# Performance work log

Hardware: AMD Instinct MI355X
Metric: run time of the kernel (lower is better)

The kernel has to match this reference:

```python
import jax, jax.numpy as jnp
import numpy as np
from jax import lax

B, T, E, H, V = 1024, 128, 300, 100, 50000
K = 4  # topk in catch()
NEG_INF = -1e30


def setup_inputs() -> dict:
    key = jax.random.key(0)
    ks = jax.random.split(key, 12)
    word_id = jax.random.randint(ks[0], (B, T), 0, V, dtype=jnp.int32)
    sen_len = jax.random.randint(ks[1], (B,), K, T + 1, dtype=jnp.int32)  # >= K for topk
    label_word_id = jax.random.randint(ks[2], (B, 1), 0, V, dtype=jnp.int32)
    emb = jax.random.normal(ks[3], (V, E), jnp.float32) * 0.1
    W_ih = jax.random.normal(ks[4], (4 * H, E), jnp.float32) * 0.05
    W_hh = jax.random.normal(ks[5], (4 * H, H), jnp.float32) * 0.05
    b_ih = jax.random.normal(ks[6], (4 * H,), jnp.float32) * 0.05
    b_hh = jax.random.normal(ks[7], (4 * H,), jnp.float32) * 0.05
    lin_W = jax.random.normal(ks[8], (6, H), jnp.float32) * 0.1
    lin_b = jax.random.normal(ks[9], (6,), jnp.float32) * 0.1
    ll_W = jax.random.normal(ks[10], (H, E), jnp.float32) * 0.05
    ll_b = jax.random.normal(ks[11], (H,), jnp.float32) * 0.05
    return dict(word_id=word_id, sen_len=sen_len, label_word_id=label_word_id,
                emb=emb, W_ih=W_ih, W_hh=W_hh, b_ih=b_ih, b_hh=b_hh,
                lin_W=lin_W, lin_b=lin_b, ll_W=ll_W, ll_b=ll_b)


def _lstm(x, W_ih, W_hh, b_ih, b_hh):
    # x: (B, T, E) -> out: (B, T, H). Single layer, pytorch gate order i,f,g,o.
    b = b_ih + b_hh
    def step(carry, x_t):
        h, c = carry
        gates = x_t @ W_ih.T + h @ W_hh.T + b  # (B, 4H)
        i, f, g, o = jnp.split(gates, 4, axis=-1)
        c = jax.nn.sigmoid(f) * c + jax.nn.sigmoid(i) * jnp.tanh(g)
        h = jax.nn.sigmoid(o) * jnp.tanh(c)
        return (h, c), h
    h0 = jnp.zeros((x.shape[0], W_hh.shape[1]), x.dtype)
    (_, _), hs = lax.scan(step, (h0, h0), x.transpose(1, 0, 2))
    return hs.transpose(1, 0, 2)


def reference(word_id, sen_len, label_word_id, emb, W_ih, W_hh, b_ih, b_hh,
              lin_W, lin_b, ll_W, ll_b):
    word_vec = emb[word_id]                      # (B, T, E)
    out = _lstm(word_vec, W_ih, W_hh, b_ih, b_hh)  # (B, T, H)

    # last valid hidden state -> linear
    last = out[jnp.arange(out.shape[0]), sen_len - 1]  # (B, H)
    out_f = last @ lin_W.T + lin_b               # (B, 6)

    # label vector through llinear
    label_vec = emb[label_word_id[:, 0]] @ ll_W.T + ll_b  # (B, H)

    # --- catch(), vectorized ---
    scores = jnp.einsum('bth,bh->bt', out, label_vec)     # (B, T)
    valid = jnp.arange(out.shape[1])[None, :] < sen_len[:, None]  # (B, T)
    vals, idx = lax.top_k(jnp.where(valid, scores, NEG_INF), K)   # (B, K)
    s_value = jnp.take_along_axis(out, idx[:, :, None], axis=1)   # (B, K, H)
    pos = jnp.sum(s_value * vals[:, :, None], axis=1)             # (B, H)

    # neg: valid positions excluding topk; original bug: vector_list accumulates
    # across the batch loop -> cumulative sum over batch dimension.
    top_mask = jnp.zeros(valid.shape, bool).at[
        jnp.arange(valid.shape[0])[:, None], idx].set(True)
    neg_mask = valid & ~top_mask                                   # (B, T)
    per_neg = jnp.einsum('bth,bt->bh', out, neg_mask.astype(out.dtype))
    neg = jnp.cumsum(per_neg, axis=0)                              # (B, H)

    l_rep = pos @ lin_W.T + lin_b
    r_rep = neg @ lin_W.T + lin_b
    return (out_f, l_rep, r_rep)
```

## Files before the change

### kernel.cpp

```cpp
#include <hip/hip_runtime.h>
#include <hip/hip_bf16.h>
#include <cstdint>

#define Bn   1024
#define Tn   128
#define En   300
#define Hn   100
#define Vn   50000
#define G4n  400
#define MPn  50048
#define NPn  448

typedef __bf16 bf16x8 __attribute__((ext_vector_type(8)));
typedef _Float16 half8 __attribute__((ext_vector_type(8)));
typedef _Float16 half2v __attribute__((ext_vector_type(2)));
typedef float  f32x4  __attribute__((ext_vector_type(4)));

#define OFF_TABLE  0ull
#define OFF_WFRAG  44800000ull
#define OFF_WFRAGB 44914688ull
#define OFF_PN6    45201408ull

__device__ __forceinline__ float sigf(float x) {
    return __builtin_amdgcn_rcpf(1.0f + __expf(-x));
}
__device__ __forceinline__ float tanhfast(float x) {
    return 1.0f - 2.0f * __builtin_amdgcn_rcpf(__expf(2.0f * x) + 1.0f);
}

#define BAR_LDS() do {                                         \
    asm volatile("s_waitcnt lgkmcnt(0)" ::: "memory");          \
    __builtin_amdgcn_s_barrier();                               \
    asm volatile("" ::: "memory");                              \
} while (0)

#define DPP_ADD_SHL(v, N) do {                                                     \
    int _s = __builtin_amdgcn_update_dpp(0, __builtin_bit_cast(int, (v)),          \
                                         0x100 | (N), 0xF, 0xF, true);             \
    (v) += __builtin_bit_cast(float, _s);                                          \
} while (0)

__global__ void k_prep(const float* __restrict__ W_ih, const float* __restrict__ W_hh,
                       uint4* __restrict__ wfrag, uint4* __restrict__ wfragB) {
    int idx = blockIdx.x * 256 + threadIdx.x;
    if (idx < 28 * 4 * 64) {
        int lane = idx & 63, tk = idx >> 6;
        int nt = tk >> 2, kc = tk & 3;
        int n = nt * 16 + (lane & 15);
        int k0 = kc * 32 + (lane >> 4) * 8;
        int q = n & 3, u = n >> 2;
        union { _Float16 h[8]; uint4 v; } pk;
#pragma unroll
        for (int j = 0; j < 8; j++) {
            int k = k0 + j;
            pk.h[j] = (_Float16)((u < Hn && k < Hn) ? W_hh[(size_t)(q * Hn + u) * Hn + k] : 0.0f);
        }
        wfrag[idx] = pk.v;
    }
    if (idx < 10 * 28 * 64) {
        int lane = idx & 63, tk = idx >> 6;
        int kc = tk / 28, nsg = tk - kc * 28;
        int n = nsg * 16 + (lane & 15);
        int k0 = kc * 32 + (lane >> 4) * 8;
        int q = n & 3, u = n >> 2;
        union { __bf16 h[8]; uint4 v; } pk;
#pragma unroll
        for (int j = 0; j < 8; j++) {
            int k = k0 + j;
            pk.h[j] = (__bf16)((u < Hn && k < En) ? W_ih[(size_t)(q * Hn + u) * En + k] : 0.0f);
        }
        wfragB[idx] = pk.v;
    }
}

__global__ __launch_bounds__(256, 2) void k_table(
    const float* __restrict__ emb, const uint4* __restrict__ wfragB,
    const float* __restrict__ b_ih, const float* __restrict__ b_hh,
    _Float16* __restrict__ table) {
    __shared__ __bf16 a_sh[64][328];
    const int tid = threadIdx.x;
    const int mt = blockIdx.x >> 1, nh = blockIdx.x & 1;

#pragma unroll
    for (int it = 0; it < 5; it++) {
        int x = it * 256 + tid;
        int row = x / 20, seg = x - row * 20;
        int gr = mt * 64 + row;
        const float* ar = emb + (size_t)(gr < Vn ? gr : Vn - 1) * En;
        int c0 = seg * 16;
        union { __bf16 h[16]; bf16x8 v[2]; } pk;
#pragma unroll
        for (int g = 0; g < 4; g++) {
            int c = c0 + g * 4;
            if (c + 4 <= En) {
                float4 f = *(const float4*)(ar + c);
                pk.h[g * 4 + 0] = (__bf16)f.x; pk.h[g * 4 + 1] = (__bf16)f.y;
                pk.h[g * 4 + 2] = (__bf16)f.z; pk.h[g * 4 + 3] = (__bf16)f.w;
            } else {
                pk.h[g * 4 + 0] = (__bf16)0.f; pk.h[g * 4 + 1] = (__bf16)0.f;
                pk.h[g * 4 + 2] = (__bf16)0.f; pk.h[g * 4 + 3] = (__bf16)0.f;
            }
        }
        *(bf16x8*)&a_sh[row][c0] = pk.v[0];
        *(bf16x8*)&a_sh[row][c0 + 8] = pk.v[1];
    }
    __syncthreads();

    const int wv = tid >> 6, l = tid & 63;
    const int c16 = l & 15, quad = l >> 4;
    f32x4 acc[14];
#pragma unroll
    for (int i = 0; i < 14; i++) acc[i] = (f32x4){0.f, 0.f, 0.f, 0.f};

    uint4 bcur[14];
#pragma unroll
    for (int ns = 0; ns < 14; ns++) bcur[ns] = wfragB[((0 * 28 + nh * 14 + ns) << 6) + l];

    for (int kc = 0; kc < 10; kc++) {
        uint4 bnxt[14];
        if (kc < 9) {
#pragma unroll
            for (int ns = 0; ns < 14; ns++) bnxt[ns] = wfragB[(((kc + 1) * 28 + nh * 14 + ns) << 6) + l];
        }
        bf16x8 af = *(const bf16x8*)&a_sh[wv * 16 + c16][kc * 32 + quad * 8];
#pragma unroll
        for (int ns = 0; ns < 14; ns++)
            acc[ns] = __builtin_amdgcn_mfma_f32_16x16x32_bf16(af, __builtin_bit_cast(bf16x8, bcur[ns]), acc[ns], 0, 0, 0);
        if (kc < 9) {
#pragma unroll
            for (int ns = 0; ns < 14; ns++) bcur[ns] = bnxt[ns];
        }
    }
#pragma unroll
    for (int ns = 0; ns < 14; ns++) {
        int n = (nh * 14 + ns) * 16 + c16;
        int q = n & 3, u = n >> 2;
        if (u < Hn) {
            int j = q * Hn + u;
            float bias = b_ih[j] + b_hh[j];
#pragma unroll
            for (int r = 0; r < 4; r++) {
                int m = mt * 64 + wv * 16 + quad * 4 + r;
                if (m < Vn) table[(size_t)m * NPn + n] = (_Float16)(acc[ns][r] + bias);
            }
        }
    }
}

__global__ __launch_bounds__(512, 2) void k_lstm(
    const int* __restrict__ word_id, const int* __restrict__ sen_len,
    const int* __restrict__ lwid, const float* __restrict__ emb,
    const float* __restrict__ llW, const float* __restrict__ llb,
    const _Float16* __restrict__ table, const uint4* __restrict__ wfrag,
    const float* __restrict__ linW, const float* __restrict__ linb,
    float* __restrict__ pn6, float* __restrict__ d_out) {
    __shared__ __align__(16) _Float16 h_cur[2][4][144];
    __shared__ __align__(16) _Float16 oh_lds[4][12832];
    __shared__ __align__(16) float    spw[4][Tn][16];
    __shared__ int      widc[4][Tn];
    __shared__ float    pos_sh[4][Hn];
    __shared__ float    lasth_sh[4][Hn];
    __shared__ float    neg_sh[4][Hn];
    __shared__ float    tk_val[4][4];
    __shared__ int      tk_idx[4][4];

    const int tid = threadIdx.x;
    const int w = tid >> 6, l = tid & 63;
    const int c16 = l & 15, quad = l >> 4;
    const int b0 = blockIdx.x * 4;

    for (int i = tid; i < 576; i += 512) ((uint32_t*)h_cur)[i] = 0u;
    { int imb = tid >> 7, it = tid & 127; widc[imb][it] = word_id[(b0 + imb) * Tn + it] * NPn; }

    const bool has4 = (w == 0);
    const int TB = has4 ? 0 : 4 + 3 * (w - 1);
    const int NT = has4 ? 4 : 3;

    half8 bfr[4][4];
#pragma unroll
    for (int kc = 0; kc < 4; kc++) {
        bfr[0][kc] = __builtin_bit_cast(half8, wfrag[((TB + 0) * 4 + kc) * 64 + l]);
        bfr[1][kc] = __builtin_bit_cast(half8, wfrag[((TB + 1) * 4 + kc) * 64 + l]);
        bfr[2][kc] = __builtin_bit_cast(half8, wfrag[((TB + 2) * 4 + kc) * 64 + l]);
        if (has4) bfr[3][kc] = __builtin_bit_cast(half8, wfrag[((TB + 3) * 4 + kc) * 64 + l]);
    }

    const int mb = c16 & 3, dup = c16 >> 2;
    const bool act = (dup < NT);
    const int u = (TB + dup) * 4 + quad;
    const int slen = act ? sen_len[b0 + mb] : 0;
    const _Float16* tb_u = table + u * 4;

    float lt_reg = 0.f;
    if (act) {
        const int lid = lwid[b0 + mb];
        const float* er = emb + (size_t)lid * En;
        const float* wr = llW + (size_t)u * En;
        float sx = 0.f, sy = 0.f, sz = 0.f, sw = 0.f;
        for (int k = 0; k < En; k += 4) {
            float4 e = *(const float4*)(er + k);
            float4 ww = *(const float4*)(wr + k);
            sx += e.x * ww.x; sy += e.y * ww.y;
            sz += e.z * ww.z; sw += e.w * ww.w;
        }
        lt_reg = (sx + sy) + (sz + sw) + llb[u];
    }

    __syncthreads();

    uint2 xq = {0, 0}, xq1 = {0, 0};
    if (act) {
        xq  = *(const uint2*)(tb_u + (size_t)widc[mb][0]);
        xq1 = *(const uint2*)(tb_u + (size_t)widc[mb][1]);
    }

    float c_reg = 0.f, sumh = 0.f, lasth = 0.f;
    float p_carry = 0.f;

    for (int t = 0; t < Tn; t++) {
        const _Float16* hp = &h_cur[t & 1][0][0];
        half8 hf0 = *(const half8*)(hp + (c16 & 3) * 144 + 0 * 32 + quad * 8);
        half8 hf1 = *(const half8*)(hp + (c16 & 3) * 144 + 1 * 32 + quad * 8);
        half8 hf2 = *(const half8*)(hp + (c16 & 3) * 144 + 2 * 32 + quad * 8);
        half8 hf3 = *(const half8*)(hp + (c16 & 3) * 144 + 3 * 32 + quad * 8);
        f32x4 acc0, acc1, acc2, acc3;
        acc0 = __builtin_amdgcn_mfma_f32_16x16x32_f16(bfr[0][0], hf0, (f32x4){0.f, 0.f, 0.f, 0.f}, 0, 0, 0);
        acc1 = __builtin_amdgcn_mfma_f32_16x16x32_f16(bfr[1][0], hf0, (f32x4){0.f, 0.f, 0.f, 0.f}, 0, 0, 0);
        acc2 = __builtin_amdgcn_mfma_f32_16x16x32_f16(bfr[2][0], hf0, (f32x4){0.f, 0.f, 0.f, 0.f}, 0, 0, 0);
        if (has4) acc3 = __builtin_amdgcn_mfma_f32_16x16x32_f16(bfr[3][0], hf0, (f32x4){0.f, 0.f, 0.f, 0.f}, 0, 0, 0);
        acc0 = __builtin_amdgcn_mfma_f32_16x16x32_f16(bfr[0][1], hf1, acc0, 0, 0, 0);
        acc1 = __builtin_amdgcn_mfma_f32_16x16x32_f16(bfr[1][1], hf1, acc1, 0, 0, 0);
        acc2 = __builtin_amdgcn_mfma_f32_16x16x32_f16(bfr[2][1], hf1, acc2, 0, 0, 0);
        if (has4) acc3 = __builtin_amdgcn_mfma_f32_16x16x32_f16(bfr[3][1], hf1, acc3, 0, 0, 0);
        acc0 = __builtin_amdgcn_mfma_f32_16x16x32_f16(bfr[0][2], hf2, acc0, 0, 0, 0);
        acc1 = __builtin_amdgcn_mfma_f32_16x16x32_f16(bfr[1][2], hf2, acc1, 0, 0, 0);
        acc2 = __builtin_amdgcn_mfma_f32_16x16x32_f16(bfr[2][2], hf2, acc2, 0, 0, 0);
        if (has4) acc3 = __builtin_amdgcn_mfma_f32_16x16x32_f16(bfr[3][2], hf2, acc3, 0, 0, 0);
        acc0 = __builtin_amdgcn_mfma_f32_16x16x32_f16(bfr[0][3], hf3, acc0, 0, 0, 0);
        acc1 = __builtin_amdgcn_mfma_f32_16x16x32_f16(bfr[1][3], hf3, acc1, 0, 0, 0);
        acc2 = __builtin_amdgcn_mfma_f32_16x16x32_f16(bfr[2][3], hf3, acc2, 0, 0, 0);
        if (has4) acc3 = __builtin_amdgcn_mfma_f32_16x16x32_f16(bfr[3][3], hf3, acc3, 0, 0, 0);
        {
            float pr = p_carry;
            DPP_ADD_SHL(pr, 4);
            DPP_ADD_SHL(pr, 8);
            int sw_ = __builtin_amdgcn_ds_swizzle(__builtin_bit_cast(int, pr), 0x401F);
            pr += __builtin_bit_cast(float, sw_);
            if (c16 < 4 && (quad & 1) == 0 && t > 0)
                spw[c16][t - 1][w * 2 + (quad >> 1)] = pr;
        }
        f32x4 g = acc0;
        g = (dup == 1) ? acc1 : g;
        g = (dup == 2) ? acc2 : g;
        if (has4) g = (dup == 3) ? acc3 : g;
        float p = 0.f;
        if (act) {
            half2v x01 = __builtin_bit_cast(half2v, xq.x);
            half2v x23 = __builtin_bit_cast(half2v, xq.y);
            float gi = g[0] + (float)x01.x;
            float gf = g[1] + (float)x01.y;
            float gg = g[2] + (float)x23.x;
            float go = g[3] + (float)x23.y;
            float c = sigf(gf) * c_reg + sigf(gi) * tanhfast(gg);
            c_reg = c;
            float hh = sigf(go) * tanhfast(c);
            _Float16 h16 = (_Float16)hh;
            h_cur[(t + 1) & 1][mb][u] = h16;
            oh_lds[mb][t * Hn + u] = h16;
            if (t < slen) sumh += hh;
            if (t == slen - 1) lasth = hh;
            p = hh * lt_reg;
            int tn2 = (t + 2 < Tn) ? t + 2 : Tn - 1;
            xq = xq1;
            xq1 = *(const uint2*)(tb_u + (size_t)widc[mb][tn2]);
        }
        p_carry = p;
        BAR_LDS();
    }
    {
        float pr = p_carry;
        DPP_ADD_SHL(pr, 4);
        DPP_ADD_SHL(pr, 8);
        int sw_ = __builtin_amdgcn_ds_swizzle(__builtin_bit_cast(int, pr), 0x401F);
        pr += __builtin_bit_cast(float, sw_);
        if (c16 < 4 && (quad & 1) == 0)
            spw[c16][Tn - 1][w * 2 + (quad >> 1)] = pr;
    }
    __syncthreads();
    if (w < 4) {
        int sl = sen_len[b0 + w];
        float4 a0 = *(const float4*)&spw[w][l][0];
        float4 a1 = *(const float4*)&spw[w][l][4];
        float4 a2 = *(const float4*)&spw[w][l][8];
        float4 a3 = *(const float4*)&spw[w][l][12];
        float4 c0 = *(const float4*)&spw[w][l + 64][0];
        float4 c1 = *(const float4*)&spw[w][l + 64][4];
        float4 c2 = *(const float4*)&spw[w][l + 64][8];
        float4 c3 = *(const float4*)&spw[w][l + 64][12];
        float sa = ((a0.x + a0.y + a0.z + a0.w) + (a1.x + a1.y + a1.z + a1.w))
                 + ((a2.x + a2.y + a2.z + a2.w) + (a3.x + a3.y + a3.z + a3.w));
        float sb = ((c0.x + c0.y + c0.z + c0.w) + (c1.x + c1.y + c1.z + c1.w))
                 + ((c2.x + c2.y + c2.z + c2.w) + (c3.x + c3.y + c3.z + c3.w));
        float s0 = (l < sl) ? sa : -1e30f;
        float s1 = (l + 64 < sl) ? sb : -1e30f;
        bool tk0 = false, tk1 = false;
#pragma unroll
        for (int p4 = 0; p4 < 4; p4++) {
            float v = tk0 ? -1e30f : s0;
            int ix = l;
            float v1 = tk1 ? -1e30f : s1;
            if (v1 > v) { v = v1; ix = l + 64; }
            for (int off = 32; off; off >>= 1) {
                float ov = __shfl_down(v, off, 64);
                int oi = __shfl_down(ix, off, 64);
                if (ov > v || (ov == v && oi < ix)) { v = ov; ix = oi; }
            }
            v = __shfl(v, 0, 64);
            ix = __shfl(ix, 0, 64);
            if (l == 0) { tk_val[w][p4] = v; tk_idx[w][p4] = ix; }
            if (ix == l) tk0 = true;
            if (ix == l + 64) tk1 = true;
        }
    }
    __syncthreads();
    if (act) {
        float pos = 0.f, nsum = sumh;
#pragma unroll
        for (int p4 = 0; p4 < 4; p4++) {
            int ix = tk_idx[mb][p4];
            float r = (float)oh_lds[mb][ix * Hn + u];
            pos += tk_val[mb][p4] * r;
            nsum -= r;
        }
        pos_sh[mb][u] = pos;
        lasth_sh[mb][u] = lasth;
        neg_sh[mb][u] = nsum;
    }
    __syncthreads();
    if (tid < 72) {
        int which = tid / 24, r = tid - which * 24;
        int pmb = r / 6, o = r - pmb * 6;
        const float* src = (which == 0) ? &lasth_sh[pmb][0]
                         : (which == 1) ? &pos_sh[pmb][0] : &neg_sh[pmb][0];
        float acc2 = (which == 2) ? 0.f : linb[o];
        for (int uu = 0; uu < Hn; uu++) acc2 += src[uu] * linW[o * Hn + uu];
        if (which == 0)      d_out[(b0 + pmb) * 6 + o] = acc2;
        else if (which == 1) d_out[Bn * 6 + (b0 + pmb) * 6 + o] = acc2;
        else                 pn6[(b0 + pmb) * 6 + o] = acc2;
    }
}

__global__ __launch_bounds__(1024) void k_scan6(const float* __restrict__ pn6,
                                                const float* __restrict__ linb,
                                                float* __restrict__ d_out) {
    __shared__ float wsum[16];
    __shared__ float wpre[16];
    int o = blockIdx.x, t = threadIdx.x;
    int lane = t & 63, wv = t >> 6;
    float v = pn6[t * 6 + o];
#pragma unroll
    for (int off = 1; off < 64; off <<= 1) {
        float x = __shfl_up(v, off, 64);
        if (lane >= off) v += x;
    }
    if (lane == 63) wsum[wv] = v;
    __syncthreads();
    if (t < 16) {
        float s = wsum[t];
#pragma unroll
        for (int off = 1; off < 16; off <<= 1) {
            float x = __shfl_up(s, off, 64);
            if (t >= off) s += x;
        }
        wpre[t] = s;
    }
    __syncthreads();
    float pre = wv ? wpre[wv - 1] : 0.f;
    d_out[2 * Bn * 6 + t * 6 + o] = v + pre + linb[o];
}

extern "C" void kernel_launch(void* const* d_in, const int* in_sizes, int n_in,
                              void* d_out, int out_size, void* d_ws, size_t ws_size,
                              hipStream_t stream) {
    const int*   word_id = (const int*)d_in[0];
    const int*   sen_len = (const int*)d_in[1];
    const int*   lwid    = (const int*)d_in[2];
    const float* emb     = (const float*)d_in[3];
    const float* W_ih    = (const float*)d_in[4];
    const float* W_hh    = (const float*)d_in[5];
    const float* b_ih    = (const float*)d_in[6];
    const float* b_hh    = (const float*)d_in[7];
    const float* linW    = (const float*)d_in[8];
    const float* linb    = (const float*)d_in[9];
    const float* llW     = (const float*)d_in[10];
    const float* llb     = (const float*)d_in[11];

    char* ws = (char*)d_ws;
    _Float16* table  = (_Float16*)(ws + OFF_TABLE);
    uint4*    wfrag  = (uint4*)(ws + OFF_WFRAG);
    uint4*    wfragB = (uint4*)(ws + OFF_WFRAGB);
    float*    pn6    = (float*)(ws + OFF_PN6);
    float*    outp   = (float*)d_out;

    k_prep<<<70, 256, 0, stream>>>(W_ih, W_hh, wfrag, wfragB);
    k_table<<<(MPn / 64) * 2, 256, 0, stream>>>(emb, wfragB, b_ih, b_hh, table);
    k_lstm<<<Bn / 4, 512, 0, stream>>>(word_id, sen_len, lwid, emb, llW, llb,
                                       table, wfrag, linW, linb, pn6, outp);
    k_scan6<<<6, 1024, 0, stream>>>(pn6, linb, outp);
}
```

Before: 270.0 us.

## Split LSTM recurrence into 2 sequences per 4-wave block

Each LSTM block now handles 2 batch rows with 4 waves instead of 4 rows with 8 waves, so each wave holds 6-7 weight tiles and issues more MFMAs per step. The grid doubles to 512 blocks, which fills more CUs and lowers per-step barrier cost across fewer waves. In exchange, each wave carries a longer serial MFMA chain per timestep, keeps more weight fragments in registers, and only 2 of 16 MFMA columns hold useful batch rows.

```diff
diff --git a/kernel.cpp b/kernel.cpp
--- a/kernel.cpp
+++ b/kernel.cpp
@@ -147,45 +147,45 @@
     }
 }
 
-__global__ __launch_bounds__(512, 2) void k_lstm(
+__global__ __launch_bounds__(256, 2) void k_lstm(
     const int* __restrict__ word_id, const int* __restrict__ sen_len,
     const int* __restrict__ lwid, const float* __restrict__ emb,
     const float* __restrict__ llW, const float* __restrict__ llb,
     const _Float16* __restrict__ table, const uint4* __restrict__ wfrag,
     const float* __restrict__ linW, const float* __restrict__ linb,
     float* __restrict__ pn6, float* __restrict__ d_out) {
-    __shared__ __align__(16) _Float16 h_cur[2][4][144];
-    __shared__ __align__(16) _Float16 oh_lds[4][12832];
-    __shared__ __align__(16) float    spw[4][Tn][16];
-    __shared__ int      widc[4][Tn];
-    __shared__ float    pos_sh[4][Hn];
-    __shared__ float    lasth_sh[4][Hn];
-    __shared__ float    neg_sh[4][Hn];
-    __shared__ float    tk_val[4][4];
-    __shared__ int      tk_idx[4][4];
+    __shared__ __align__(16) _Float16 h_cur[2][2][144];
+    __shared__ __align__(16) _Float16 oh_lds[2][12832];
+    __shared__ __align__(16) float    spw[2][Tn][16];
+    __shared__ int      widc[2][Tn];
+    __shared__ float    pos_sh[2][Hn];
+    __shared__ float    lasth_sh[2][Hn];
+    __shared__ float    neg_sh[2][Hn];
+    __shared__ float    tk_val[2][4];
+    __shared__ int      tk_idx[2][4];
 
     const int tid = threadIdx.x;
     const int w = tid >> 6, l = tid & 63;
     const int c16 = l & 15, quad = l >> 4;
-    const int b0 = blockIdx.x * 4;
-
-    for (int i = tid; i < 576; i += 512) ((uint32_t*)h_cur)[i] = 0u;
+    const int b0 = blockIdx.x * 2;
+
+    for (int i = tid; i < 288; i += 256) ((uint32_t*)h_cur)[i] = 0u;
     { int imb = tid >> 7, it = tid & 127; widc[imb][it] = word_id[(b0 + imb) * Tn + it] * NPn; }
 
-    const bool has4 = (w == 0);
-    const int TB = has4 ? 0 : 4 + 3 * (w - 1);
-    const int NT = has4 ? 4 : 3;
-
-    half8 bfr[4][4];
+    const bool has7 = (w == 0);
+    const int TB = has7 ? 0 : 7 + 6 * (w - 1);
+    const int NT = has7 ? 7 : 6;
+
+    half8 bfr[7][4];
 #pragma unroll
     for (int kc = 0; kc < 4; kc++) {
-        bfr[0][kc] = __builtin_bit_cast(half8, wfrag[((TB + 0) * 4 + kc) * 64 + l]);
-        bfr[1][kc] = __builtin_bit_cast(half8, wfrag[((TB + 1) * 4 + kc) * 64 + l]);
-        bfr[2][kc] = __builtin_bit_cast(half8, wfrag[((TB + 2) * 4 + kc) * 64 + l]);
-        if (has4) bfr[3][kc] = __builtin_bit_cast(half8, wfrag[((TB + 3) * 4 + kc) * 64 + l]);
-    }
-
-    const int mb = c16 & 3, dup = c16 >> 2;
+#pragma unroll
+        for (int i = 0; i < 6; i++)
+            bfr[i][kc] = __builtin_bit_cast(half8, wfrag[((TB + i) * 4 + kc) * 64 + l]);
+        if (has7) bfr[6][kc] = __builtin_bit_cast(half8, wfrag[((TB + 6) * 4 + kc) * 64 + l]);
+    }
+
+    const int mb = c16 & 1, dup = c16 >> 1;
     const bool act = (dup < NT);
     const int u = (TB + dup) * 4 + quad;
     const int slen = act ? sen_len[b0 + mb] : 0;
@@ -219,40 +219,38 @@
 
     for (int t = 0; t < Tn; t++) {
         const _Float16* hp = &h_cur[t & 1][0][0];
-        half8 hf0 = *(const half8*)(hp + (c16 & 3) * 144 + 0 * 32 + quad * 8);
-        half8 hf1 = *(const half8*)(hp + (c16 & 3) * 144 + 1 * 32 + quad * 8);
-        half8 hf2 = *(const half8*)(hp + (c16 & 3) * 144 + 2 * 32 + quad * 8);
-        half8 hf3 = *(const half8*)(hp + (c16 & 3) * 144 + 3 * 32 + quad * 8);
-        f32x4 acc0, acc1, acc2, acc3;
-        acc0 = __builtin_amdgcn_mfma_f32_16x16x32_f16(bfr[0][0], hf0, (f32x4){0.f, 0.f, 0.f, 0.f}, 0, 0, 0);
-        acc1 = __builtin_amdgcn_mfma_f32_16x16x32_f16(bfr[1][0], hf0, (f32x4){0.f, 0.f, 0.f, 0.f}, 0, 0, 0);
-        acc2 = __builtin_amdgcn_mfma_f32_16x16x32_f16(bfr[2][0], hf0, (f32x4){0.f, 0.f, 0.f, 0.f}, 0, 0, 0);
-        if (has4) acc3 = __builtin_amdgcn_mfma_f32_16x16x32_f16(bfr[3][0], hf0, (f32x4){0.f, 0.f, 0.f, 0.f}, 0, 0, 0);
-        acc0 = __builtin_amdgcn_mfma_f32_16x16x32_f16(bfr[0][1], hf1, acc0, 0, 0, 0);
-        acc1 = __builtin_amdgcn_mfma_f32_16x16x32_f16(bfr[1][1], hf1, acc1, 0, 0, 0);
-        acc2 = __builtin_amdgcn_mfma_f32_16x16x32_f16(bfr[2][1], hf1, acc2, 0, 0, 0);
-        if (has4) acc3 = __builtin_amdgcn_mfma_f32_16x16x32_f16(bfr[3][1], hf1, acc3, 0, 0, 0);
-        acc0 = __builtin_amdgcn_mfma_f32_16x16x32_f16(bfr[0][2], hf2, acc0, 0, 0, 0);
-        acc1 = __builtin_amdgcn_mfma_f32_16x16x32_f16(bfr[1][2], hf2, acc1, 0, 0, 0);
-        acc2 = __builtin_amdgcn_mfma_f32_16x16x32_f16(bfr[2][2], hf2, acc2, 0, 0, 0);
-        if (has4) acc3 = __builtin_amdgcn_mfma_f32_16x16x32_f16(bfr[3][2], hf2, acc3, 0, 0, 0);
-        acc0 = __builtin_amdgcn_mfma_f32_16x16x32_f16(bfr[0][3], hf3, acc0, 0, 0, 0);
-        acc1 = __builtin_amdgcn_mfma_f32_16x16x32_f16(bfr[1][3], hf3, acc1, 0, 0, 0);
-        acc2 = __builtin_amdgcn_mfma_f32_16x16x32_f16(bfr[2][3], hf3, acc2, 0, 0, 0);
-        if (has4) acc3 = __builtin_amdgcn_mfma_f32_16x16x32_f16(bfr[3][3], hf3, acc3, 0, 0, 0);
+        f32x4 acc[7];
+#pragma unroll
+        for (int kc = 0; kc < 4; kc++) {
+            half8 hf = *(const half8*)(hp + (c16 & 1) * 144 + kc * 32 + quad * 8);
+            if (kc == 0) {
+#pragma unroll
+                for (int i = 0; i < 6; i++)
+                    acc[i] = __builtin_amdgcn_mfma_f32_16x16x32_f16(bfr[i][0], hf, (f32x4){0.f, 0.f, 0.f, 0.f}, 0, 0, 0);
+                if (has7)
+                    acc[6] = __builtin_amdgcn_mfma_f32_16x16x32_f16(bfr[6][0], hf, (f32x4){0.f, 0.f, 0.f, 0.f}, 0, 0, 0);
+            } else {
+#pragma unroll
+                for (int i = 0; i < 6; i++)
+                    acc[i] = __builtin_amdgcn_mfma_f32_16x16x32_f16(bfr[i][kc], hf, acc[i], 0, 0, 0);
+                if (has7)
+                    acc[6] = __builtin_amdgcn_mfma_f32_16x16x32_f16(bfr[6][kc], hf, acc[6], 0, 0, 0);
+            }
+        }
         {
             float pr = p_carry;
+            DPP_ADD_SHL(pr, 2);
             DPP_ADD_SHL(pr, 4);
             DPP_ADD_SHL(pr, 8);
-            int sw_ = __builtin_amdgcn_ds_swizzle(__builtin_bit_cast(int, pr), 0x401F);
-            pr += __builtin_bit_cast(float, sw_);
-            if (c16 < 4 && (quad & 1) == 0 && t > 0)
-                spw[c16][t - 1][w * 2 + (quad >> 1)] = pr;
-        }
-        f32x4 g = acc0;
-        g = (dup == 1) ? acc1 : g;
-        g = (dup == 2) ? acc2 : g;
-        if (has4) g = (dup == 3) ? acc3 : g;
+            if (c16 < 2 && t > 0) spw[c16][t - 1][w * 4 + quad] = pr;
+        }
+        f32x4 g = acc[0];
+        g = (dup == 1) ? acc[1] : g;
+        g = (dup == 2) ? acc[2] : g;
+        g = (dup == 3) ? acc[3] : g;
+        g = (dup == 4) ? acc[4] : g;
+        g = (dup == 5) ? acc[5] : g;
+        if (has7) g = (dup == 6) ? acc[6] : g;
         float p = 0.f;
         if (act) {
             half2v x01 = __builtin_bit_cast(half2v, xq.x);
@@ -279,15 +277,13 @@
     }
     {
         float pr = p_carry;
+        DPP_ADD_SHL(pr, 2);
         DPP_ADD_SHL(pr, 4);
         DPP_ADD_SHL(pr, 8);
-        int sw_ = __builtin_amdgcn_ds_swizzle(__builtin_bit_cast(int, pr), 0x401F);
-        pr += __builtin_bit_cast(float, sw_);
-        if (c16 < 4 && (quad & 1) == 0)
-            spw[c16][Tn - 1][w * 2 + (quad >> 1)] = pr;
-    }
-    __syncthreads();
-    if (w < 4) {
+        if (c16 < 2) spw[c16][Tn - 1][w * 4 + quad] = pr;
+    }
+    __syncthreads();
+    if (w < 2) {
         int sl = sen_len[b0 + w];
         float4 a0 = *(const float4*)&spw[w][l][0];
         float4 a1 = *(const float4*)&spw[w][l][4];
@@ -337,8 +333,8 @@
         neg_sh[mb][u] = nsum;
     }
     __syncthreads();
-    if (tid < 72) {
-        int which = tid / 24, r = tid - which * 24;
+    if (tid < 36) {
+        int which = tid / 12, r = tid - which * 12;
         int pmb = r / 6, o = r - pmb * 6;
         const float* src = (which == 0) ? &lasth_sh[pmb][0]
                          : (which == 1) ? &pos_sh[pmb][0] : &neg_sh[pmb][0];
@@ -404,7 +400,7 @@
 
     k_prep<<<70, 256, 0, stream>>>(W_ih, W_hh, wfrag, wfragB);
     k_table<<<(MPn / 64) * 2, 256, 0, stream>>>(emb, wfragB, b_ih, b_hh, table);
-    k_lstm<<<Bn / 4, 512, 0, stream>>>(word_id, sen_len, lwid, emb, llW, llb,
+    k_lstm<<<Bn / 2, 256, 0, stream>>>(word_id, sen_len, lwid, emb, llW, llb,
                                        table, wfrag, linW, linb, pn6, outp);
     k_scan6<<<6, 1024, 0, stream>>>(pn6, linb, outp);
 }
```

Measured after the change: 277.7 us. 1.03x slower.
